# Optimization experiments

Measured on AMD Instinct MI355X. Metric: run time of the kernel, lower is better.

The kernel has to match this reference:

```python
import jax, jax.numpy as jnp
import numpy as np

NH = 16  # num_attention_heads
DH = 64  # attention_head_size
HID = NH * DH
TYPE_VOCAB = 2


def setup_inputs() -> dict:
    key = jax.random.key(0)
    ks = jax.random.split(key, 10)
    B, S = 4, 2048
    s = 0.02
    return {
        "hidden_states": jax.random.normal(ks[0], (B, S, HID), jnp.float32),
        "attention_mask": jnp.zeros((B, 1, 1, S), jnp.float32),
        "seg_ids": jax.random.randint(ks[1], (B, S), 0, TYPE_VOCAB),
        "Wq": jax.random.normal(ks[2], (HID, HID), jnp.float32) * s,
        "bq": jnp.zeros((HID,), jnp.float32),
        "Wk": jax.random.normal(ks[3], (HID, HID), jnp.float32) * s,  # key has NO bias (F.linear with weight only)
        "Wv": jax.random.normal(ks[4], (HID, HID), jnp.float32) * s,
        "bv": jnp.zeros((HID,), jnp.float32),
        "seg_table": jax.random.normal(ks[5], (TYPE_VOCAB, HID), jnp.float32) * s,
        "b_q_s": jnp.zeros((1, NH, 1, DH), jnp.float32),
    }


def reference(hidden_states, attention_mask, seg_ids, Wq, bq, Wk, Wv, bv, seg_table, b_q_s):
    B, S, H = hidden_states.shape
    # QKV projections (key projection has no bias, matching F.linear(x, key.weight))
    q = hidden_states @ Wq.T + bq
    k = hidden_states @ Wk.T
    v = hidden_states @ Wv.T + bv
    # [B, NH, S, DH]
    q = q.reshape(B, S, NH, DH).transpose(0, 2, 1, 3)
    k = k.reshape(B, S, NH, DH).transpose(0, 2, 1, 3)
    v = v.reshape(B, S, NH, DH).transpose(0, 2, 1, 3)
    scale = 1.0 / np.sqrt(DH).astype(np.float32)
    scores = jnp.einsum('bhid,bhjd->bhij', q * scale, k)
    # segment-embedding bias: seg_rep [B, S, NH, DH]
    seg_rep = seg_table[seg_ids].reshape(B, S, NH, DH)
    qs = jnp.einsum('bhid,bjhd->bhij', q + b_q_s, seg_rep)
    scores = scores + qs + attention_mask
    probs = jax.nn.softmax(scores, axis=-1)  # dropout: eval mode (identity)
    ctx = jnp.einsum('bhij,bhjd->bihd', probs, v).reshape(B, S, H)
    return ctx
```

## Files before the change

kernel.cpp:

```cpp
#include <hip/hip_runtime.h>
#include <cstdint>
#include <cmath>

#define RLN2 1.44269504088896340736f

typedef __attribute__((ext_vector_type(8))) short short8;
typedef __attribute__((ext_vector_type(4))) float f32x4;
typedef __attribute__((ext_vector_type(16))) float f32x16;
typedef __attribute__((ext_vector_type(4))) unsigned int uint4v;

__device__ __forceinline__ unsigned short f2bf(float f) {
  unsigned int u = __float_as_uint(f);
  u += 0x7fffu + ((u >> 16) & 1u);
  return (unsigned short)(u >> 16);
}

__device__ __forceinline__ unsigned int cvt_pk_bf16(float lo, float hi) {
  unsigned int r;
  asm("v_cvt_pk_bf16_f32 %0, %1, %2" : "=v"(r) : "v"(lo), "v"(hi));
  return r;
}

__device__ __forceinline__ float fast_exp2(float x) {
#if __has_builtin(__builtin_amdgcn_exp2f)
  return __builtin_amdgcn_exp2f(x);
#else
  return exp2f(x);
#endif
}

__device__ __forceinline__ void gload16(const void* g, void* l) {
  __builtin_amdgcn_global_load_lds(
      (const __attribute__((address_space(1))) unsigned int*)g,
      (__attribute__((address_space(3))) unsigned int*)l,
      16, 0, 0);
}


__global__ void __launch_bounds__(256) k_cvt_hs(const float* __restrict__ src,
                                                unsigned short* __restrict__ dst) {
  size_t i = (size_t)blockIdx.x * 256 + threadIdx.x;
  const float4* s = (const float4*)src + i * 2;
  float4 a = s[0], b = s[1];
  short8 o;
  o[0] = (short)f2bf(a.x); o[1] = (short)f2bf(a.y); o[2] = (short)f2bf(a.z); o[3] = (short)f2bf(a.w);
  o[4] = (short)f2bf(b.x); o[5] = (short)f2bf(b.y); o[6] = (short)f2bf(b.z); o[7] = (short)f2bf(b.w);
  ((short8*)dst)[i] = o;
}

__global__ void __launch_bounds__(256) k_cvt_w(const float* __restrict__ Wq,
                                               const float* __restrict__ Wk,
                                               const float* __restrict__ Wv,
                                               unsigned short* __restrict__ dst) {
  size_t i = (size_t)blockIdx.x * 256 + threadIdx.x;
  int e = (int)(i * 8);
  int n = e >> 10, c = e & 1023;
  const float* row = (n < 1024) ? (Wq + (size_t)n * 1024)
                   : (n < 2048) ? (Wk + (size_t)(n - 1024) * 1024)
                                : (Wv + (size_t)(n - 2048) * 1024);
  const float4* s = (const float4*)(row + c);
  float4 a = s[0], b = s[1];
  short8 o;
  o[0] = (short)f2bf(a.x); o[1] = (short)f2bf(a.y); o[2] = (short)f2bf(a.z); o[3] = (short)f2bf(a.w);
  o[4] = (short)f2bf(b.x); o[5] = (short)f2bf(b.y); o[6] = (short)f2bf(b.z); o[7] = (short)f2bf(b.w);
  ((short8*)dst)[i] = o;
}

__global__ void __launch_bounds__(256) k_seg(const int* __restrict__ seg_ids,
                                             const float* __restrict__ seg_table,
                                             unsigned short* __restrict__ Kaug) {
  size_t i = (size_t)blockIdx.x * 256 + threadIdx.x;
  int e = (int)(i * 8);
  int jl = e >> 10;
  int r  = e & 1023;
  int sid = seg_ids[jl];
  const float4* s = (const float4*)(seg_table + (size_t)sid * 1024 + r);
  float4 a = s[0], b = s[1];
  short8 o;
  o[0] = (short)f2bf(a.x); o[1] = (short)f2bf(a.y); o[2] = (short)f2bf(a.z); o[3] = (short)f2bf(a.w);
  o[4] = (short)f2bf(b.x); o[5] = (short)f2bf(b.y); o[6] = (short)f2bf(b.z); o[7] = (short)f2bf(b.w);
  int b_ = jl >> 11, j = jl & 2047;
  int h = r >> 6, d = r & 63;
  size_t off = ((size_t)(b_ * 16 + h) * 2048 + j) * 128 + 64 + d;
  *(short8*)(Kaug + off) = o;
}

__global__ void __launch_bounds__(256) k_vt(const unsigned short* __restrict__ V,
                                            unsigned short* __restrict__ Vt) {
  __shared__ unsigned short lt[64 * 72];
  int blk = blockIdx.x;
  int bh = blk >> 5, jt = blk & 31;
  int j0 = jt * 64;
  int tid = threadIdx.x;
  const char* src = (const char*)(V + ((size_t)bh * 2048 + j0) * 64);
#pragma unroll
  for (int it = 0; it < 2; ++it) {
    int c = tid + it * 256;
    int j = c >> 3, colb = (c & 7) * 16;
    int kh2 = (j >> 5) & 1, c2 = (j >> 3) & 3, hi2 = (j >> 2) & 1, r2 = j & 3;
    int jpos = (2 * kh2 + (c2 >> 1)) * 16 + 8 * hi2 + 4 * (c2 & 1) + r2;
    short8 v = *(const short8*)(src + (size_t)j * 128 + colb);
    int d0 = colb >> 1;
#pragma unroll
    for (int e = 0; e < 8; ++e)
      lt[(d0 + e) * 72 + jpos] = (unsigned short)v[e];
  }
  __syncthreads();
  char* dst = (char*)(Vt + (size_t)bh * 131072 + j0);
#pragma unroll
  for (int it = 0; it < 2; ++it) {
    int c = tid + it * 256;
    int d = c >> 3, jc = (c & 7) * 8;
    short8 o = *(const short8*)&lt[d * 72 + jc];
    *(short8*)(dst + (size_t)d * 4096 + jc * 2) = o;
  }
}

__global__ void __launch_bounds__(256) k_gemm(const unsigned short* __restrict__ A,
                                              const unsigned short* __restrict__ Bw,
                                              const float* __restrict__ bq,
                                              const float* __restrict__ bv,
                                              const float* __restrict__ bqs,
                                              unsigned short* __restrict__ Qaug,
                                              unsigned short* __restrict__ Kaug,
                                              unsigned short* __restrict__ Vo) {
  __shared__ unsigned short As[128 * 32];
  __shared__ unsigned short Bs[128 * 32];
  int n0 = blockIdx.x * 128;
  int m0 = blockIdx.y * 128;
  int tid = threadIdx.x;
  int w = tid >> 6, lane = tid & 63;
  int wr = (w >> 1) * 64, wc = (w & 1) * 64;
  int rA = lane & 15;
  int kg = (lane >> 4) * 16;
  f32x4 acc[4][4] = {};
  const char* Ab = (const char*)A;
  const char* Bb = (const char*)Bw;

  for (int kt = 0; kt < 32; ++kt) {
    int kb0 = kt * 64;
#pragma unroll
    for (int c = 0; c < 2; ++c) {
      int chunk = w * 2 + c;
      int y = chunk * 1024 + lane * 16;
      int row = y >> 6, colb = y & 63;
      gload16(Ab + (size_t)(m0 + row) * 2048 + kb0 + colb, (char*)As + chunk * 1024);
      gload16(Bb + (size_t)(n0 + row) * 2048 + kb0 + colb, (char*)Bs + chunk * 1024);
    }
    __syncthreads();
    short8 af[4], bfr[4];
#pragma unroll
    for (int m = 0; m < 4; ++m)
      af[m] = *(const short8*)((const char*)As + (wr + m * 16 + rA) * 64 + kg);
#pragma unroll
    for (int n = 0; n < 4; ++n)
      bfr[n] = *(const short8*)((const char*)Bs + (wc + n * 16 + rA) * 64 + kg);
#pragma unroll
    for (int m = 0; m < 4; ++m)
#pragma unroll
      for (int n = 0; n < 4; ++n)
        acc[m][n] = __builtin_amdgcn_mfma_f32_16x16x32_bf16(af[m], bfr[n], acc[m][n], 0, 0, 0);
    __syncthreads();
  }

  int seg = n0 >> 10;
  int colbase = n0 & 1023;
#pragma unroll
  for (int n = 0; n < 4; ++n) {
    int o = colbase + wc + n * 16 + (lane & 15);
    int h = o >> 6, d = o & 63;
    float bias = 0.f, bqsv = 0.f;
    if (seg == 0) { bias = bq[o]; bqsv = bqs[o]; }
    else if (seg == 2) { bias = bv[o]; }
#pragma unroll
    for (int m = 0; m < 4; ++m) {
#pragma unroll
      for (int r = 0; r < 4; ++r) {
        int i = m0 + wr + m * 16 + (lane >> 4) * 4 + r;
        int b_ = i >> 11, sdx = i & 2047;
        float val = acc[m][n][r];
        size_t tok = (size_t)(b_ * 16 + h) * 2048 + sdx;
        if (seg == 0) {
          float qv = val + bias;
          Qaug[tok * 128 + d]      = f2bf(qv * (0.125f * RLN2));
          Qaug[tok * 128 + 64 + d] = f2bf((qv + bqsv) * RLN2);
        } else if (seg == 1) {
          Kaug[tok * 128 + d] = f2bf(val);
        } else {
          Vo[tok * 64 + d] = f2bf(val + bias);
        }
      }
    }
  }
}

__global__ void __launch_bounds__(256, 3) k_attn(const unsigned short* __restrict__ Qaug,
                                                 const unsigned short* __restrict__ Kaug,
                                                 const unsigned short* __restrict__ Vt,
                                                 const float* __restrict__ mask,
                                                 float* __restrict__ out) {
  __shared__ char smem[49152];
  char* Ksb = smem;
  char* Vsb = smem + 32768;

  int qt = blockIdx.x, h = blockIdx.y, b_ = blockIdx.z;
  int bh = b_ * 16 + h;
  int i0 = qt * 128;
  int tid = threadIdx.x, w = tid >> 6, lane = tid & 63;
  int q = lane & 31, hi = lane >> 5;
  int swzq = (q & 7) << 4;
  const char* Qg = (const char*)Qaug + (size_t)bh * 2048 * 256;
  const char* Kg = (const char*)Kaug + (size_t)bh * 2048 * 256;
  const char* Vg = (const char*)Vt + (size_t)bh * 64 * 4096;
  const float* maskb = mask + (size_t)b_ * 2048;

  int foff[8];
#pragma unroll
  for (int ds = 0; ds < 8; ++ds)
    foff[ds] = (ds * 32 + hi * 16) ^ swzq;

  int kst_row = lane >> 4, kst_x = (lane & 15) * 16;
  int vst_dv = lane >> 3;
  int vst_x = ((lane & 7) * 16) ^ ((vst_dv & 7) << 4);

#pragma unroll
  for (int c = 0; c < 4; ++c) {
    int ck = w * 4 + c;
    int krow = ck * 4 + kst_row;
    gload16(Kg + (size_t)krow * 256 + (kst_x ^ ((krow & 7) << 4)), Ksb + ck * 1024);
  }
#pragma unroll
  for (int c = 0; c < 2; ++c) {
    int ck = w * 2 + c;
    int dv = ck * 8 + vst_dv;
    gload16(Vg + (size_t)dv * 4096 + vst_x, Vsb + ck * 1024);
  }

  short8 qf[8];
  {
    const char* qrow = Qg + (size_t)(i0 + w * 32 + q) * 256 + hi * 16;
#pragma unroll
    for (int ds = 0; ds < 8; ++ds)
      qf[ds] = *(const short8*)(qrow + ds * 32);
  }
  __syncthreads();

  float m_run = -1e30f, l_run = 0.f;
  f32x16 accO[2] = {};

  for (int t = 0; t < 32; ++t) {
    int cur = t & 1, nxt = cur ^ 1;
    int j0 = t * 64;
    if (t < 31) {
      int jn = j0 + 64;
      char* kd = Ksb + nxt * 16384;
      char* vd = Vsb + nxt * 8192;
#pragma unroll
      for (int c = 0; c < 4; ++c) {
        int ck = w * 4 + c;
        int krow = ck * 4 + kst_row;
        gload16(Kg + (size_t)(jn + krow) * 256 + (kst_x ^ ((krow & 7) << 4)), kd + ck * 1024);
      }
#pragma unroll
      for (int c = 0; c < 2; ++c) {
        int ck = w * 2 + c;
        int dv = ck * 8 + vst_dv;
        gload16(Vg + (size_t)dv * 4096 + jn * 2 + vst_x, vd + ck * 1024);
      }
    }
    const char* kq = Ksb + cur * 16384 + q * 256;
    const char* vq = Vsb + cur * 8192 + q * 128;

    f32x16 s0 = {}, s1 = {};
    __builtin_amdgcn_s_setprio(1);
#pragma unroll
    for (int ds = 0; ds < 8; ++ds) {
      short8 kf0 = *(const short8*)(kq + foff[ds]);
      short8 kf1 = *(const short8*)(kq + foff[ds] + 8192);
      s0 = __builtin_amdgcn_mfma_f32_32x32x16_bf16(kf0, qf[ds], s0, 0, 0, 0);
      s1 = __builtin_amdgcn_mfma_f32_32x32x16_bf16(kf1, qf[ds], s1, 0, 0, 0);
    }
    __builtin_amdgcn_s_setprio(0);

#pragma unroll
    for (int c = 0; c < 4; ++c) {
      f32x4 mv0 = *(const f32x4*)(maskb + j0 + 8 * c + 4 * hi);
      f32x4 mv1 = *(const f32x4*)(maskb + j0 + 32 + 8 * c + 4 * hi);
#pragma unroll
      for (int r = 0; r < 4; ++r) {
        s0[4 * c + r] += mv0[r] * RLN2;
        s1[4 * c + r] += mv1[r] * RLN2;
      }
    }

    float tm = -1e30f;
#pragma unroll
    for (int i = 0; i < 16; ++i) tm = fmaxf(tm, fmaxf(s0[i], s1[i]));
    tm = fmaxf(tm, __shfl_xor(tm, 32));

    if (__any(tm > m_run + 8.0f)) {
      float mn = fmaxf(m_run, tm);
      float alpha = fast_exp2(m_run - mn);
      m_run = mn;
      l_run *= alpha;
#pragma unroll
      for (int i = 0; i < 16; ++i) { accO[0][i] *= alpha; accO[1][i] *= alpha; }
    }

    float ps = 0.f;
#pragma unroll
    for (int i = 0; i < 16; ++i) {
      float e0 = fast_exp2(s0[i] - m_run);
      float e1 = fast_exp2(s1[i] - m_run);
      s0[i] = e0; s1[i] = e1;
      ps += e0 + e1;
    }
    ps += __shfl_xor(ps, 32);
    l_run += ps;

    uint4v pk[4];
#pragma unroll
    for (int ks = 0; ks < 4; ++ks) {
      int o = 8 * (ks & 1);
      const f32x16& sv = (ks < 2) ? s0 : s1;
      pk[ks][0] = cvt_pk_bf16(sv[o + 0], sv[o + 1]);
      pk[ks][1] = cvt_pk_bf16(sv[o + 2], sv[o + 3]);
      pk[ks][2] = cvt_pk_bf16(sv[o + 4], sv[o + 5]);
      pk[ks][3] = cvt_pk_bf16(sv[o + 6], sv[o + 7]);
    }

    __builtin_amdgcn_s_setprio(1);
#pragma unroll
    for (int ks = 0; ks < 4; ++ks) {
      short8 pf = __builtin_bit_cast(short8, pk[ks]);
      short8 vf0 = *(const short8*)(vq + foff[ks]);
      short8 vf1 = *(const short8*)(vq + foff[ks] + 4096);
      accO[0] = __builtin_amdgcn_mfma_f32_32x32x16_bf16(vf0, pf, accO[0], 0, 0, 0);
      accO[1] = __builtin_amdgcn_mfma_f32_32x32x16_bf16(vf1, pf, accO[1], 0, 0, 0);
    }
    __builtin_amdgcn_s_setprio(0);
    __syncthreads();
  }

  float inv = 1.0f / l_run;
  float* orow = out + ((size_t)b_ * 2048 + i0 + w * 32 + q) * 1024 + h * 64;
#pragma unroll
  for (int vh = 0; vh < 2; ++vh) {
#pragma unroll
    for (int c = 0; c < 4; ++c) {
      f32x4 o;
      o[0] = accO[vh][4 * c + 0] * inv;
      o[1] = accO[vh][4 * c + 1] * inv;
      o[2] = accO[vh][4 * c + 2] * inv;
      o[3] = accO[vh][4 * c + 3] * inv;
      *(f32x4*)(orow + vh * 32 + 8 * c + 4 * hi) = o;
    }
  }
}

extern "C" void kernel_launch(void* const* d_in, const int* in_sizes, int n_in,
                              void* d_out, int out_size, void* d_ws, size_t ws_size,
                              hipStream_t stream) {
  (void)in_sizes; (void)n_in; (void)out_size; (void)ws_size;
  const float* hs        = (const float*)d_in[0];
  const float* mask      = (const float*)d_in[1];
  const int*   seg_ids   = (const int*)d_in[2];
  const float* Wq        = (const float*)d_in[3];
  const float* bq        = (const float*)d_in[4];
  const float* Wk        = (const float*)d_in[5];
  const float* Wv        = (const float*)d_in[6];
  const float* bv        = (const float*)d_in[7];
  const float* seg_table = (const float*)d_in[8];
  const float* bqs       = (const float*)d_in[9];
  float* out = (float*)d_out;
  char* ws = (char*)d_ws;

  unsigned short* hsb  = (unsigned short*)(ws + 0);
  unsigned short* Wcat = (unsigned short*)(ws + 16777216);
  unsigned short* Qaug = (unsigned short*)(ws + 23068672);
  unsigned short* Kaug = (unsigned short*)(ws + 56623104);
  unsigned short* V    = (unsigned short*)(ws + 90177536);
  unsigned short* Vt   = (unsigned short*)(ws + 0);

  k_cvt_hs<<<dim3(4096), dim3(256), 0, stream>>>(hs, hsb);
  k_cvt_w<<<dim3(1536), dim3(256), 0, stream>>>(Wq, Wk, Wv, Wcat);
  k_gemm<<<dim3(24, 64), dim3(256), 0, stream>>>(hsb, Wcat, bq, bv, bqs, Qaug, Kaug, V);
  k_seg<<<dim3(4096), dim3(256), 0, stream>>>(seg_ids, seg_table, Kaug);
  k_vt<<<dim3(2048), dim3(256), 0, stream>>>(V, Vt);
  k_attn<<<dim3(16, 16, 4), dim3(256), 0, stream>>>(Qaug, Kaug, Vt, mask, out);
}
```

Measured before the change: 280.4 us.

## Fuse V transpose into GEMM epilogue and double query rows per attention block

The QKV GEMM epilogue now writes V straight into the permuted transposed layout the attention kernel expects, which removes the separate transpose kernel and its round trip through memory. The attention kernel now handles 256 query rows per block, with each wave processing two 32-row query groups. Each K/V tile loaded into shared memory is therefore reused across twice as many queries, and the grid is halved. The cost is more registers per thread (launch bounds drop from 3 to 2 blocks per SIMD), fewer blocks to spread across the GPU, and scattered 8-byte V stores in the GEMM epilogue.

```diff
diff --git a/kernel.cpp b/kernel.cpp
--- a/kernel.cpp
+++ b/kernel.cpp
@@ -5,6 +5,7 @@
 #define RLN2 1.44269504088896340736f
 
 typedef __attribute__((ext_vector_type(8))) short short8;
+typedef __attribute__((ext_vector_type(4))) short short4v;
 typedef __attribute__((ext_vector_type(4))) float f32x4;
 typedef __attribute__((ext_vector_type(16))) float f32x16;
 typedef __attribute__((ext_vector_type(4))) unsigned int uint4v;
@@ -85,37 +86,6 @@
   *(short8*)(Kaug + off) = o;
 }
 
-__global__ void __launch_bounds__(256) k_vt(const unsigned short* __restrict__ V,
-                                            unsigned short* __restrict__ Vt) {
-  __shared__ unsigned short lt[64 * 72];
-  int blk = blockIdx.x;
-  int bh = blk >> 5, jt = blk & 31;
-  int j0 = jt * 64;
-  int tid = threadIdx.x;
-  const char* src = (const char*)(V + ((size_t)bh * 2048 + j0) * 64);
-#pragma unroll
-  for (int it = 0; it < 2; ++it) {
-    int c = tid + it * 256;
-    int j = c >> 3, colb = (c & 7) * 16;
-    int kh2 = (j >> 5) & 1, c2 = (j >> 3) & 3, hi2 = (j >> 2) & 1, r2 = j & 3;
-    int jpos = (2 * kh2 + (c2 >> 1)) * 16 + 8 * hi2 + 4 * (c2 & 1) + r2;
-    short8 v = *(const short8*)(src + (size_t)j * 128 + colb);
-    int d0 = colb >> 1;
-#pragma unroll
-    for (int e = 0; e < 8; ++e)
-      lt[(d0 + e) * 72 + jpos] = (unsigned short)v[e];
-  }
-  __syncthreads();
-  char* dst = (char*)(Vt + (size_t)bh * 131072 + j0);
-#pragma unroll
-  for (int it = 0; it < 2; ++it) {
-    int c = tid + it * 256;
-    int d = c >> 3, jc = (c & 7) * 8;
-    short8 o = *(const short8*)&lt[d * 72 + jc];
-    *(short8*)(dst + (size_t)d * 4096 + jc * 2) = o;
-  }
-}
-
 __global__ void __launch_bounds__(256) k_gemm(const unsigned short* __restrict__ A,
                                               const unsigned short* __restrict__ Bw,
                                               const float* __restrict__ bq,
@@ -123,7 +93,7 @@
                                               const float* __restrict__ bqs,
                                               unsigned short* __restrict__ Qaug,
                                               unsigned short* __restrict__ Kaug,
-                                              unsigned short* __restrict__ Vo) {
+                                              unsigned short* __restrict__ Vt) {
   __shared__ unsigned short As[128 * 32];
   __shared__ unsigned short Bs[128 * 32];
   int n0 = blockIdx.x * 128;
@@ -165,6 +135,7 @@
 
   int seg = n0 >> 10;
   int colbase = n0 & 1023;
+  int g = lane >> 4;
 #pragma unroll
   for (int n = 0; n < 4; ++n) {
     int o = colbase + wc + n * 16 + (lane & 15);
@@ -174,27 +145,37 @@
     else if (seg == 2) { bias = bv[o]; }
 #pragma unroll
     for (int m = 0; m < 4; ++m) {
-#pragma unroll
-      for (int r = 0; r < 4; ++r) {
-        int i = m0 + wr + m * 16 + (lane >> 4) * 4 + r;
+      if (seg == 2) {
+        int i = m0 + wr + m * 16 + g * 4;
         int b_ = i >> 11, sdx = i & 2047;
-        float val = acc[m][n][r];
-        size_t tok = (size_t)(b_ * 16 + h) * 2048 + sdx;
-        if (seg == 0) {
-          float qv = val + bias;
-          Qaug[tok * 128 + d]      = f2bf(qv * (0.125f * RLN2));
-          Qaug[tok * 128 + 64 + d] = f2bf((qv + bqsv) * RLN2);
-        } else if (seg == 1) {
-          Kaug[tok * 128 + d] = f2bf(val);
-        } else {
-          Vo[tok * 64 + d] = f2bf(val + bias);
+        int bh = b_ * 16 + h;
+        int pos = (sdx & ~63) + 32 * ((m >> 1) & 1) + 16 * (m & 1) + 8 * (g & 1) + 4 * ((g >> 1) & 1);
+        short4v pv;
+#pragma unroll
+        for (int r = 0; r < 4; ++r)
+          pv[r] = (short)f2bf(acc[m][n][r] + bias);
+        *(short4v*)(Vt + (size_t)bh * 131072 + (size_t)d * 2048 + pos) = pv;
+      } else {
+#pragma unroll
+        for (int r = 0; r < 4; ++r) {
+          int i = m0 + wr + m * 16 + g * 4 + r;
+          int b_ = i >> 11, sdx = i & 2047;
+          float val = acc[m][n][r];
+          size_t tok = (size_t)(b_ * 16 + h) * 2048 + sdx;
+          if (seg == 0) {
+            float qv = val + bias;
+            Qaug[tok * 128 + d]      = f2bf(qv * (0.125f * RLN2));
+            Qaug[tok * 128 + 64 + d] = f2bf((qv + bqsv) * RLN2);
+          } else {
+            Kaug[tok * 128 + d] = f2bf(val);
+          }
         }
       }
     }
   }
 }
 
-__global__ void __launch_bounds__(256, 3) k_attn(const unsigned short* __restrict__ Qaug,
+__global__ void __launch_bounds__(256, 2) k_attn(const unsigned short* __restrict__ Qaug,
                                                  const unsigned short* __restrict__ Kaug,
                                                  const unsigned short* __restrict__ Vt,
                                                  const float* __restrict__ mask,
@@ -205,7 +186,7 @@
 
   int qt = blockIdx.x, h = blockIdx.y, b_ = blockIdx.z;
   int bh = b_ * 16 + h;
-  int i0 = qt * 128;
+  int i0 = qt * 256;
   int tid = threadIdx.x, w = tid >> 6, lane = tid & 63;
   int q = lane & 31, hi = lane >> 5;
   int swzq = (q & 7) << 4;
@@ -236,17 +217,20 @@
     gload16(Vg + (size_t)dv * 4096 + vst_x, Vsb + ck * 1024);
   }
 
-  short8 qf[8];
+  short8 qfA[8], qfB[8];
   {
-    const char* qrow = Qg + (size_t)(i0 + w * 32 + q) * 256 + hi * 16;
-#pragma unroll
-    for (int ds = 0; ds < 8; ++ds)
-      qf[ds] = *(const short8*)(qrow + ds * 32);
+    const char* qrowA = Qg + (size_t)(i0 + w * 64 + q) * 256 + hi * 16;
+    const char* qrowB = qrowA + 32 * 256;
+#pragma unroll
+    for (int ds = 0; ds < 8; ++ds) {
+      qfA[ds] = *(const short8*)(qrowA + ds * 32);
+      qfB[ds] = *(const short8*)(qrowB + ds * 32);
+    }
   }
   __syncthreads();
 
-  float m_run = -1e30f, l_run = 0.f;
-  f32x16 accO[2] = {};
+  float mA = -1e30f, lA = 0.f, mB = -1e30f, lB = 0.f;
+  f32x16 accA0 = {}, accA1 = {}, accB0 = {}, accB1 = {};
 
   for (int t = 0; t < 32; ++t) {
     int cur = t & 1, nxt = cur ^ 1;
@@ -271,14 +255,16 @@
     const char* kq = Ksb + cur * 16384 + q * 256;
     const char* vq = Vsb + cur * 8192 + q * 128;
 
-    f32x16 s0 = {}, s1 = {};
+    f32x16 sA0 = {}, sA1 = {}, sB0 = {}, sB1 = {};
     __builtin_amdgcn_s_setprio(1);
 #pragma unroll
     for (int ds = 0; ds < 8; ++ds) {
       short8 kf0 = *(const short8*)(kq + foff[ds]);
       short8 kf1 = *(const short8*)(kq + foff[ds] + 8192);
-      s0 = __builtin_amdgcn_mfma_f32_32x32x16_bf16(kf0, qf[ds], s0, 0, 0, 0);
-      s1 = __builtin_amdgcn_mfma_f32_32x32x16_bf16(kf1, qf[ds], s1, 0, 0, 0);
+      sA0 = __builtin_amdgcn_mfma_f32_32x32x16_bf16(kf0, qfA[ds], sA0, 0, 0, 0);
+      sB0 = __builtin_amdgcn_mfma_f32_32x32x16_bf16(kf0, qfB[ds], sB0, 0, 0, 0);
+      sA1 = __builtin_amdgcn_mfma_f32_32x32x16_bf16(kf1, qfA[ds], sA1, 0, 0, 0);
+      sB1 = __builtin_amdgcn_mfma_f32_32x32x16_bf16(kf1, qfB[ds], sB1, 0, 0, 0);
     }
     __builtin_amdgcn_s_setprio(0);
 
@@ -288,73 +274,104 @@
       f32x4 mv1 = *(const f32x4*)(maskb + j0 + 32 + 8 * c + 4 * hi);
 #pragma unroll
       for (int r = 0; r < 4; ++r) {
-        s0[4 * c + r] += mv0[r] * RLN2;
-        s1[4 * c + r] += mv1[r] * RLN2;
-      }
-    }
-
-    float tm = -1e30f;
-#pragma unroll
-    for (int i = 0; i < 16; ++i) tm = fmaxf(tm, fmaxf(s0[i], s1[i]));
-    tm = fmaxf(tm, __shfl_xor(tm, 32));
-
-    if (__any(tm > m_run + 8.0f)) {
-      float mn = fmaxf(m_run, tm);
-      float alpha = fast_exp2(m_run - mn);
-      m_run = mn;
-      l_run *= alpha;
-#pragma unroll
-      for (int i = 0; i < 16; ++i) { accO[0][i] *= alpha; accO[1][i] *= alpha; }
-    }
-
-    float ps = 0.f;
-#pragma unroll
-    for (int i = 0; i < 16; ++i) {
-      float e0 = fast_exp2(s0[i] - m_run);
-      float e1 = fast_exp2(s1[i] - m_run);
-      s0[i] = e0; s1[i] = e1;
-      ps += e0 + e1;
-    }
-    ps += __shfl_xor(ps, 32);
-    l_run += ps;
-
-    uint4v pk[4];
+        float a0 = mv0[r] * RLN2, a1 = mv1[r] * RLN2;
+        sA0[4 * c + r] += a0; sB0[4 * c + r] += a0;
+        sA1[4 * c + r] += a1; sB1[4 * c + r] += a1;
+      }
+    }
+
+    {
+      float tm = -1e30f;
+#pragma unroll
+      for (int i = 0; i < 16; ++i) tm = fmaxf(tm, fmaxf(sA0[i], sA1[i]));
+      tm = fmaxf(tm, __shfl_xor(tm, 32));
+      if (__any(tm > mA + 8.0f)) {
+        float mn = fmaxf(mA, tm);
+        float alpha = fast_exp2(mA - mn);
+        mA = mn; lA *= alpha;
+#pragma unroll
+        for (int i = 0; i < 16; ++i) { accA0[i] *= alpha; accA1[i] *= alpha; }
+      }
+      float ps = 0.f;
+#pragma unroll
+      for (int i = 0; i < 16; ++i) {
+        float e0 = fast_exp2(sA0[i] - mA);
+        float e1 = fast_exp2(sA1[i] - mA);
+        sA0[i] = e0; sA1[i] = e1;
+        ps += e0 + e1;
+      }
+      ps += __shfl_xor(ps, 32);
+      lA += ps;
+    }
+    {
+      float tm = -1e30f;
+#pragma unroll
+      for (int i = 0; i < 16; ++i) tm = fmaxf(tm, fmaxf(sB0[i], sB1[i]));
+      tm = fmaxf(tm, __shfl_xor(tm, 32));
+      if (__any(tm > mB + 8.0f)) {
+        float mn = fmaxf(mB, tm);
+        float alpha = fast_exp2(mB - mn);
+        mB = mn; lB *= alpha;
+#pragma unroll
+        for (int i = 0; i < 16; ++i) { accB0[i] *= alpha; accB1[i] *= alpha; }
+      }
+      float ps = 0.f;
+#pragma unroll
+      for (int i = 0; i < 16; ++i) {
+        float e0 = fast_exp2(sB0[i] - mB);
+        float e1 = fast_exp2(sB1[i] - mB);
+        sB0[i] = e0; sB1[i] = e1;
+        ps += e0 + e1;
+      }
+      ps += __shfl_xor(ps, 32);
+      lB += ps;
+    }
+
+    __builtin_amdgcn_s_setprio(1);
 #pragma unroll
     for (int ks = 0; ks < 4; ++ks) {
       int o = 8 * (ks & 1);
-      const f32x16& sv = (ks < 2) ? s0 : s1;
-      pk[ks][0] = cvt_pk_bf16(sv[o + 0], sv[o + 1]);
-      pk[ks][1] = cvt_pk_bf16(sv[o + 2], sv[o + 3]);
-      pk[ks][2] = cvt_pk_bf16(sv[o + 4], sv[o + 5]);
-      pk[ks][3] = cvt_pk_bf16(sv[o + 6], sv[o + 7]);
-    }
-
-    __builtin_amdgcn_s_setprio(1);
-#pragma unroll
-    for (int ks = 0; ks < 4; ++ks) {
-      short8 pf = __builtin_bit_cast(short8, pk[ks]);
+      const f32x16& svA = (ks < 2) ? sA0 : sA1;
+      const f32x16& svB = (ks < 2) ? sB0 : sB1;
+      uint4v pa, pb;
+      pa[0] = cvt_pk_bf16(svA[o + 0], svA[o + 1]);
+      pa[1] = cvt_pk_bf16(svA[o + 2], svA[o + 3]);
+      pa[2] = cvt_pk_bf16(svA[o + 4], svA[o + 5]);
+      pa[3] = cvt_pk_bf16(svA[o + 6], svA[o + 7]);
+      pb[0] = cvt_pk_bf16(svB[o + 0], svB[o + 1]);
+      pb[1] = cvt_pk_bf16(svB[o + 2], svB[o + 3]);
+      pb[2] = cvt_pk_bf16(svB[o + 4], svB[o + 5]);
+      pb[3] = cvt_pk_bf16(svB[o + 6], svB[o + 7]);
+      short8 pfA = __builtin_bit_cast(short8, pa);
+      short8 pfB = __builtin_bit_cast(short8, pb);
       short8 vf0 = *(const short8*)(vq + foff[ks]);
       short8 vf1 = *(const short8*)(vq + foff[ks] + 4096);
-      accO[0] = __builtin_amdgcn_mfma_f32_32x32x16_bf16(vf0, pf, accO[0], 0, 0, 0);
-      accO[1] = __builtin_amdgcn_mfma_f32_32x32x16_bf16(vf1, pf, accO[1], 0, 0, 0);
+      accA0 = __builtin_amdgcn_mfma_f32_32x32x16_bf16(vf0, pfA, accA0, 0, 0, 0);
+      accB0 = __builtin_amdgcn_mfma_f32_32x32x16_bf16(vf0, pfB, accB0, 0, 0, 0);
+      accA1 = __builtin_amdgcn_mfma_f32_32x32x16_bf16(vf1, pfA, accA1, 0, 0, 0);
+      accB1 = __builtin_amdgcn_mfma_f32_32x32x16_bf16(vf1, pfB, accB1, 0, 0, 0);
     }
     __builtin_amdgcn_s_setprio(0);
     __syncthreads();
   }
 
-  float inv = 1.0f / l_run;
-  float* orow = out + ((size_t)b_ * 2048 + i0 + w * 32 + q) * 1024 + h * 64;
-#pragma unroll
-  for (int vh = 0; vh < 2; ++vh) {
-#pragma unroll
-    for (int c = 0; c < 4; ++c) {
-      f32x4 o;
-      o[0] = accO[vh][4 * c + 0] * inv;
-      o[1] = accO[vh][4 * c + 1] * inv;
-      o[2] = accO[vh][4 * c + 2] * inv;
-      o[3] = accO[vh][4 * c + 3] * inv;
-      *(f32x4*)(orow + vh * 32 + 8 * c + 4 * hi) = o;
-    }
+  float invA = 1.0f / lA, invB = 1.0f / lB;
+  float* orowA = out + ((size_t)b_ * 2048 + i0 + w * 64 + q) * 1024 + h * 64;
+  float* orowB = orowA + 32 * 1024;
+#pragma unroll
+  for (int c = 0; c < 4; ++c) {
+    f32x4 oa0, oa1, ob0, ob1;
+#pragma unroll
+    for (int r = 0; r < 4; ++r) {
+      oa0[r] = accA0[4 * c + r] * invA;
+      oa1[r] = accA1[4 * c + r] * invA;
+      ob0[r] = accB0[4 * c + r] * invB;
+      ob1[r] = accB1[4 * c + r] * invB;
+    }
+    *(f32x4*)(orowA + 8 * c + 4 * hi)      = oa0;
+    *(f32x4*)(orowA + 32 + 8 * c + 4 * hi) = oa1;
+    *(f32x4*)(orowB + 8 * c + 4 * hi)      = ob0;
+    *(f32x4*)(orowB + 32 + 8 * c + 4 * hi) = ob1;
   }
 }
 
@@ -379,13 +396,11 @@
   unsigned short* Wcat = (unsigned short*)(ws + 16777216);
   unsigned short* Qaug = (unsigned short*)(ws + 23068672);
   unsigned short* Kaug = (unsigned short*)(ws + 56623104);
-  unsigned short* V    = (unsigned short*)(ws + 90177536);
-  unsigned short* Vt   = (unsigned short*)(ws + 0);
+  unsigned short* Vt   = (unsigned short*)(ws + 90177536);
 
   k_cvt_hs<<<dim3(4096), dim3(256), 0, stream>>>(hs, hsb);
   k_cvt_w<<<dim3(1536), dim3(256), 0, stream>>>(Wq, Wk, Wv, Wcat);
-  k_gemm<<<dim3(24, 64), dim3(256), 0, stream>>>(hsb, Wcat, bq, bv, bqs, Qaug, Kaug, V);
+  k_gemm<<<dim3(24, 64), dim3(256), 0, stream>>>(hsb, Wcat, bq, bv, bqs, Qaug, Kaug, Vt);
   k_seg<<<dim3(4096), dim3(256), 0, stream>>>(seg_ids, seg_table, Kaug);
-  k_vt<<<dim3(2048), dim3(256), 0, stream>>>(V, Vt);
-  k_attn<<<dim3(16, 16, 4), dim3(256), 0, stream>>>(Qaug, Kaug, Vt, mask, out);
-}
+  k_attn<<<dim3(8, 16, 4), dim3(256), 0, stream>>>(Qaug, Kaug, Vt, mask, out);
+}
```

After: 289.7 us. 1.03x slower.

## Write V in MFMA fragment layout from GEMM and read it directly in attention

Applied to the files above, without the earlier changes.

The QKV GEMM epilogue now stores V as bf16 short4 vectors in a pre-blocked layout that matches the B-operand fragment order of the PV MFMA. This removes the separate V-transpose kernel and lets attention load V fragments straight from global memory instead of staging them through LDS. Freeing that LDS lets the kernel raise its occupancy hint from 3 to 4 blocks. The grid is also flattened so that blocks sharing a query tile across heads are adjacent. The cost is uncached global V loads inside the inner loop, which rely on L2 hits and could stall the MFMA pipeline.

```diff
diff --git a/kernel.cpp b/kernel.cpp
--- a/kernel.cpp
+++ b/kernel.cpp
@@ -5,6 +5,7 @@
 #define RLN2 1.44269504088896340736f
 
 typedef __attribute__((ext_vector_type(8))) short short8;
+typedef __attribute__((ext_vector_type(4))) short short4v;
 typedef __attribute__((ext_vector_type(4))) float f32x4;
 typedef __attribute__((ext_vector_type(16))) float f32x16;
 typedef __attribute__((ext_vector_type(4))) unsigned int uint4v;
@@ -85,37 +86,6 @@
   *(short8*)(Kaug + off) = o;
 }
 
-__global__ void __launch_bounds__(256) k_vt(const unsigned short* __restrict__ V,
-                                            unsigned short* __restrict__ Vt) {
-  __shared__ unsigned short lt[64 * 72];
-  int blk = blockIdx.x;
-  int bh = blk >> 5, jt = blk & 31;
-  int j0 = jt * 64;
-  int tid = threadIdx.x;
-  const char* src = (const char*)(V + ((size_t)bh * 2048 + j0) * 64);
-#pragma unroll
-  for (int it = 0; it < 2; ++it) {
-    int c = tid + it * 256;
-    int j = c >> 3, colb = (c & 7) * 16;
-    int kh2 = (j >> 5) & 1, c2 = (j >> 3) & 3, hi2 = (j >> 2) & 1, r2 = j & 3;
-    int jpos = (2 * kh2 + (c2 >> 1)) * 16 + 8 * hi2 + 4 * (c2 & 1) + r2;
-    short8 v = *(const short8*)(src + (size_t)j * 128 + colb);
-    int d0 = colb >> 1;
-#pragma unroll
-    for (int e = 0; e < 8; ++e)
-      lt[(d0 + e) * 72 + jpos] = (unsigned short)v[e];
-  }
-  __syncthreads();
-  char* dst = (char*)(Vt + (size_t)bh * 131072 + j0);
-#pragma unroll
-  for (int it = 0; it < 2; ++it) {
-    int c = tid + it * 256;
-    int d = c >> 3, jc = (c & 7) * 8;
-    short8 o = *(const short8*)&lt[d * 72 + jc];
-    *(short8*)(dst + (size_t)d * 4096 + jc * 2) = o;
-  }
-}
-
 __global__ void __launch_bounds__(256) k_gemm(const unsigned short* __restrict__ A,
                                               const unsigned short* __restrict__ Bw,
                                               const float* __restrict__ bq,
@@ -123,7 +93,7 @@
                                               const float* __restrict__ bqs,
                                               unsigned short* __restrict__ Qaug,
                                               unsigned short* __restrict__ Kaug,
-                                              unsigned short* __restrict__ Vo) {
+                                              unsigned short* __restrict__ Vb) {
   __shared__ unsigned short As[128 * 32];
   __shared__ unsigned short Bs[128 * 32];
   int n0 = blockIdx.x * 128;
@@ -165,6 +135,7 @@
 
   int seg = n0 >> 10;
   int colbase = n0 & 1023;
+  int g = lane >> 4;
 #pragma unroll
   for (int n = 0; n < 4; ++n) {
     int o = colbase + wc + n * 16 + (lane & 15);
@@ -174,44 +145,55 @@
     else if (seg == 2) { bias = bv[o]; }
 #pragma unroll
     for (int m = 0; m < 4; ++m) {
-#pragma unroll
-      for (int r = 0; r < 4; ++r) {
-        int i = m0 + wr + m * 16 + (lane >> 4) * 4 + r;
+      if (seg == 2) {
+        int i = m0 + wr + m * 16 + g * 4;
         int b_ = i >> 11, sdx = i & 2047;
-        float val = acc[m][n][r];
-        size_t tok = (size_t)(b_ * 16 + h) * 2048 + sdx;
-        if (seg == 0) {
-          float qv = val + bias;
-          Qaug[tok * 128 + d]      = f2bf(qv * (0.125f * RLN2));
-          Qaug[tok * 128 + 64 + d] = f2bf((qv + bqsv) * RLN2);
-        } else if (seg == 1) {
-          Kaug[tok * 128 + d] = f2bf(val);
-        } else {
-          Vo[tok * 64 + d] = f2bf(val + bias);
+        int bh = b_ * 16 + h;
+        int jblk = (sdx >> 6) * 4 + 2 * ((m >> 1) & 1) + (m & 1);
+        int kk = 8 * (g & 1) + 4 * ((g >> 1) & 1);
+        short4v pv;
+#pragma unroll
+        for (int r = 0; r < 4; ++r)
+          pv[r] = (short)f2bf(acc[m][n][r] + bias);
+        *(short4v*)(Vb + (size_t)bh * 131072 + jblk * 1024 + d * 16 + kk) = pv;
+      } else {
+#pragma unroll
+        for (int r = 0; r < 4; ++r) {
+          int i = m0 + wr + m * 16 + g * 4 + r;
+          int b_ = i >> 11, sdx = i & 2047;
+          float val = acc[m][n][r];
+          size_t tok = (size_t)(b_ * 16 + h) * 2048 + sdx;
+          if (seg == 0) {
+            float qv = val + bias;
+            Qaug[tok * 128 + d]      = f2bf(qv * (0.125f * RLN2));
+            Qaug[tok * 128 + 64 + d] = f2bf((qv + bqsv) * RLN2);
+          } else {
+            Kaug[tok * 128 + d] = f2bf(val);
+          }
         }
       }
     }
   }
 }
 
-__global__ void __launch_bounds__(256, 3) k_attn(const unsigned short* __restrict__ Qaug,
+__global__ void __launch_bounds__(256, 4) k_attn(const unsigned short* __restrict__ Qaug,
                                                  const unsigned short* __restrict__ Kaug,
-                                                 const unsigned short* __restrict__ Vt,
+                                                 const unsigned short* __restrict__ Vb,
                                                  const float* __restrict__ mask,
                                                  float* __restrict__ out) {
-  __shared__ char smem[49152];
+  __shared__ char smem[32768];
   char* Ksb = smem;
-  char* Vsb = smem + 32768;
-
-  int qt = blockIdx.x, h = blockIdx.y, b_ = blockIdx.z;
-  int bh = b_ * 16 + h;
+
+  int bid = blockIdx.x;
+  int bh = bid & 63, qt = bid >> 6;
+  int h = bh & 15, b_ = bh >> 4;
   int i0 = qt * 128;
   int tid = threadIdx.x, w = tid >> 6, lane = tid & 63;
   int q = lane & 31, hi = lane >> 5;
   int swzq = (q & 7) << 4;
   const char* Qg = (const char*)Qaug + (size_t)bh * 2048 * 256;
   const char* Kg = (const char*)Kaug + (size_t)bh * 2048 * 256;
-  const char* Vg = (const char*)Vt + (size_t)bh * 64 * 4096;
+  const char* Vbg = (const char*)Vb + (size_t)bh * 262144;
   const float* maskb = mask + (size_t)b_ * 2048;
 
   int foff[8];
@@ -219,21 +201,15 @@
   for (int ds = 0; ds < 8; ++ds)
     foff[ds] = (ds * 32 + hi * 16) ^ swzq;
 
+  const char* vbl = Vbg + (lane & 31) * 32 + hi * 16;
+
   int kst_row = lane >> 4, kst_x = (lane & 15) * 16;
-  int vst_dv = lane >> 3;
-  int vst_x = ((lane & 7) * 16) ^ ((vst_dv & 7) << 4);
 
 #pragma unroll
   for (int c = 0; c < 4; ++c) {
     int ck = w * 4 + c;
     int krow = ck * 4 + kst_row;
     gload16(Kg + (size_t)krow * 256 + (kst_x ^ ((krow & 7) << 4)), Ksb + ck * 1024);
-  }
-#pragma unroll
-  for (int c = 0; c < 2; ++c) {
-    int ck = w * 2 + c;
-    int dv = ck * 8 + vst_dv;
-    gload16(Vg + (size_t)dv * 4096 + vst_x, Vsb + ck * 1024);
   }
 
   short8 qf[8];
@@ -254,22 +230,15 @@
     if (t < 31) {
       int jn = j0 + 64;
       char* kd = Ksb + nxt * 16384;
-      char* vd = Vsb + nxt * 8192;
 #pragma unroll
       for (int c = 0; c < 4; ++c) {
         int ck = w * 4 + c;
         int krow = ck * 4 + kst_row;
         gload16(Kg + (size_t)(jn + krow) * 256 + (kst_x ^ ((krow & 7) << 4)), kd + ck * 1024);
       }
-#pragma unroll
-      for (int c = 0; c < 2; ++c) {
-        int ck = w * 2 + c;
-        int dv = ck * 8 + vst_dv;
-        gload16(Vg + (size_t)dv * 4096 + jn * 2 + vst_x, vd + ck * 1024);
-      }
     }
     const char* kq = Ksb + cur * 16384 + q * 256;
-    const char* vq = Vsb + cur * 8192 + q * 128;
+    const char* vbp = vbl + t * 8192;
 
     f32x16 s0 = {}, s1 = {};
     __builtin_amdgcn_s_setprio(1);
@@ -318,23 +287,19 @@
     ps += __shfl_xor(ps, 32);
     l_run += ps;
 
-    uint4v pk[4];
+    __builtin_amdgcn_s_setprio(1);
 #pragma unroll
     for (int ks = 0; ks < 4; ++ks) {
       int o = 8 * (ks & 1);
       const f32x16& sv = (ks < 2) ? s0 : s1;
-      pk[ks][0] = cvt_pk_bf16(sv[o + 0], sv[o + 1]);
-      pk[ks][1] = cvt_pk_bf16(sv[o + 2], sv[o + 3]);
-      pk[ks][2] = cvt_pk_bf16(sv[o + 4], sv[o + 5]);
-      pk[ks][3] = cvt_pk_bf16(sv[o + 6], sv[o + 7]);
-    }
-
-    __builtin_amdgcn_s_setprio(1);
-#pragma unroll
-    for (int ks = 0; ks < 4; ++ks) {
-      short8 pf = __builtin_bit_cast(short8, pk[ks]);
-      short8 vf0 = *(const short8*)(vq + foff[ks]);
-      short8 vf1 = *(const short8*)(vq + foff[ks] + 4096);
+      uint4v pa;
+      pa[0] = cvt_pk_bf16(sv[o + 0], sv[o + 1]);
+      pa[1] = cvt_pk_bf16(sv[o + 2], sv[o + 3]);
+      pa[2] = cvt_pk_bf16(sv[o + 4], sv[o + 5]);
+      pa[3] = cvt_pk_bf16(sv[o + 6], sv[o + 7]);
+      short8 pf = __builtin_bit_cast(short8, pa);
+      short8 vf0 = *(const short8*)(vbp + ks * 2048);
+      short8 vf1 = *(const short8*)(vbp + ks * 2048 + 1024);
       accO[0] = __builtin_amdgcn_mfma_f32_32x32x16_bf16(vf0, pf, accO[0], 0, 0, 0);
       accO[1] = __builtin_amdgcn_mfma_f32_32x32x16_bf16(vf1, pf, accO[1], 0, 0, 0);
     }
@@ -379,13 +344,11 @@
   unsigned short* Wcat = (unsigned short*)(ws + 16777216);
   unsigned short* Qaug = (unsigned short*)(ws + 23068672);
   unsigned short* Kaug = (unsigned short*)(ws + 56623104);
-  unsigned short* V    = (unsigned short*)(ws + 90177536);
-  unsigned short* Vt   = (unsigned short*)(ws + 0);
+  unsigned short* Vb   = (unsigned short*)(ws + 90177536);
 
   k_cvt_hs<<<dim3(4096), dim3(256), 0, stream>>>(hs, hsb);
   k_cvt_w<<<dim3(1536), dim3(256), 0, stream>>>(Wq, Wk, Wv, Wcat);
-  k_gemm<<<dim3(24, 64), dim3(256), 0, stream>>>(hsb, Wcat, bq, bv, bqs, Qaug, Kaug, V);
+  k_gemm<<<dim3(24, 64), dim3(256), 0, stream>>>(hsb, Wcat, bq, bv, bqs, Qaug, Kaug, Vb);
   k_seg<<<dim3(4096), dim3(256), 0, stream>>>(seg_ids, seg_table, Kaug);
-  k_vt<<<dim3(2048), dim3(256), 0, stream>>>(V, Vt);
-  k_attn<<<dim3(16, 16, 4), dim3(256), 0, stream>>>(Qaug, Kaug, Vt, mask, out);
-}
+  k_attn<<<dim3(1024), dim3(256), 0, stream>>>(Qaug, Kaug, Vb, mask, out);
+}
```

After: 423.5 us. 51.0% more time.
